# Kernel optimization log

Measured on AMD Instinct MI355X. Metric: run time of the kernel, lower is better.

## Reference

```python
import jax, jax.numpy as jnp
import numpy as np

N_GRAPHS = 128
N_NODES = 512
N = N_GRAPHS * N_NODES      # 65536 total nodes
E = 524288                  # edges (avg degree 8)
F_IN = 4                    # num_features
EMB = 4                     # embedding_dim
HEADS = 4
GDIM = 16                   # GATConv_dim
D = GDIM * HEADS            # 64 = d_model
NHEAD = 2                   # heads // 2
FF = 64                     # ff_hid_dim
OUT = 64                    # output_dim
N_GAT_REST = 3              # gat_layers - 1


def setup_inputs() -> dict:
    key = jax.random.key(0)
    ks = iter(jax.random.split(key, 64))
    def nrm(shape, fan_in):
        return jax.random.normal(next(ks), shape, jnp.float32) / np.float32(np.sqrt(fan_in))
    inp = {}
    inp['x'] = jax.random.normal(next(ks), (N, F_IN), jnp.float32)
    inp['edge_index'] = jax.random.randint(next(ks), (2, E), 0, N, dtype=jnp.int32)
    inp['batch'] = jnp.repeat(jnp.arange(N_GRAPHS, dtype=jnp.int32), N_NODES)
    # feature_fc
    inp['Wf'] = nrm((F_IN, EMB), F_IN); inp['bf'] = jnp.zeros((EMB,), jnp.float32)
    # input GATConv (EMB -> HEADS*GDIM)
    inp['gW0'] = nrm((EMB, HEADS * GDIM), EMB)
    inp['aS0'] = nrm((HEADS, GDIM), GDIM); inp['aD0'] = nrm((HEADS, GDIM), GDIM)
    inp['gb0'] = jnp.zeros((D,), jnp.float32)
    # remaining 3 GATConv layers (D -> HEADS*GDIM), stacked
    inp['gW'] = nrm((N_GAT_REST, D, HEADS * GDIM), D)
    inp['aS'] = nrm((N_GAT_REST, HEADS, GDIM), GDIM); inp['aD'] = nrm((N_GAT_REST, HEADS, GDIM), GDIM)
    inp['gb'] = jnp.zeros((N_GAT_REST, D), jnp.float32)
    # decoder layer: self-attn, cross-attn, layernorms, FFN
    for p in ['sWq','sWk','sWv','sWo','cWq','cWk','cWv','cWo']:
        inp[p] = nrm((D, D), D)
    for p in ['sbq','sbk','sbv','sbo','cbq','cbk','cbv','cbo']:
        inp[p] = jnp.zeros((D,), jnp.float32)
    for g, b in [('ln1g','ln1b'), ('ln2g','ln2b'), ('ln3g','ln3b')]:
        inp[g] = jnp.ones((D,), jnp.float32); inp[b] = jnp.zeros((D,), jnp.float32)
    inp['ffW1'] = nrm((D, FF), D); inp['ffb1'] = jnp.zeros((FF,), jnp.float32)
    inp['ffW2'] = nrm((FF, D), FF); inp['ffb2'] = jnp.zeros((D,), jnp.float32)
    inp['fcW'] = nrm((D, OUT), D); inp['fcb'] = jnp.zeros((OUT,), jnp.float32)
    return inp


def _gat(h_in, src, dst, W, a_s, a_d, b):
    # PyG GATConv, concat=True, negative_slope=0.2, self-loops already in (src,dst)
    h = (h_in @ W).reshape(N, HEADS, GDIM)
    es = jnp.einsum('nho,ho->nh', h, a_s)   # [N,H]
    ed = jnp.einsum('nho,ho->nh', h, a_d)
    e = jax.nn.leaky_relu(es[src] + ed[dst], 0.2)          # [E',H]
    m = jax.ops.segment_max(e, dst, num_segments=N)        # segment softmax over dst
    w = jnp.exp(e - m[dst])
    s = jax.ops.segment_sum(w, dst, num_segments=N)
    alpha = w / (s[dst] + 1e-16)
    out = jax.ops.segment_sum(h[src] * alpha[..., None], dst, num_segments=N)
    return out.reshape(N, D) + b


def _mha(q, kv, Wq, bq, Wk, bk, Wv, bv, Wo, bo):
    B, S, Dm = q.shape
    hd = Dm // NHEAD
    Q = (q @ Wq + bq).reshape(B, S, NHEAD, hd)
    K = (kv @ Wk + bk).reshape(B, S, NHEAD, hd)
    V = (kv @ Wv + bv).reshape(B, S, NHEAD, hd)
    a = jax.nn.softmax(jnp.einsum('bqhd,bkhd->bhqk', Q, K) / jnp.sqrt(jnp.float32(hd)), axis=-1)
    o = jnp.einsum('bhqk,bkhd->bqhd', a, V).reshape(B, S, Dm)
    return o @ Wo + bo


def _ln(x, g, b):
    m = x.mean(-1, keepdims=True)
    v = ((x - m) ** 2).mean(-1, keepdims=True)
    return (x - m) / jnp.sqrt(v + 1e-5) * g + b


def reference(x, edge_index, batch, Wf, bf, gW0, aS0, aD0, gb0, gW, aS, aD, gb,
              sWq, sWk, sWv, sWo, cWq, cWk, cWv, cWo,
              sbq, sbk, sbv, sbo, cbq, cbk, cbv, cbo,
              ln1g, ln1b, ln2g, ln2b, ln3g, ln3b,
              ffW1, ffb1, ffW2, ffb2, fcW, fcb):
    loops = jnp.arange(N, dtype=edge_index.dtype)
    src = jnp.concatenate([edge_index[0], loops])
    dst = jnp.concatenate([edge_index[1], loops])
    h = x @ Wf + bf
    h = jax.nn.leaky_relu(_gat(h, src, dst, gW0, aS0, aD0, gb0), 0.01)
    for i in range(N_GAT_REST):
        h = jax.nn.leaky_relu(_gat(h, src, dst, gW[i], aS[i], aD[i], gb[i]), 0.01)
    t = h.reshape(N_GRAPHS, N_NODES, D)
    # one transformer decoder layer, post-norm, memory = layer input
    mem = t
    t = _ln(t + _mha(t, t, sWq, sbq, sWk, sbk, sWv, sbv, sWo, sbo), ln1g, ln1b)
    t = _ln(t + _mha(t, mem, cWq, cbq, cWk, cbk, cWv, cbv, cWo, cbo), ln2g, ln2b)
    t = _ln(t + (jax.nn.relu(t @ ffW1 + ffb1) @ ffW2 + ffb2), ln3g, ln3b)
    h = t.reshape(N, D)
    pooled = jax.ops.segment_sum(h, batch, num_segments=N_GRAPHS) / jnp.float32(N_NODES)
    return pooled @ fcW + fcb
```

## Files before the change

### kernel.cpp

```cpp
#include <hip/hip_runtime.h>
#include <math.h>

#define NG 128
#define SEQ 512
#define NN 65536
#define EE 524288
#define DM 64

typedef __attribute__((ext_vector_type(8))) short short8;
typedef __attribute__((ext_vector_type(4))) float f32x4;

__device__ __forceinline__ float lrelu(float x, float s){ return x > 0.f ? x : s*x; }

__device__ __forceinline__ unsigned short f2bf(float x){
  union { float f; unsigned u; } v; v.f = x;
  unsigned r = v.u + 0x7FFF + ((v.u>>16)&1);
  return (unsigned short)(r>>16);
}
__device__ __forceinline__ float bf2f(unsigned short x){
  union { unsigned u; float f; } v; v.u = ((unsigned)x)<<16;
  return v.f;
}

__global__ void k_count(const int* __restrict__ dst, int* __restrict__ deg){
  int e = blockIdx.x*256 + threadIdx.x;
  atomicAdd(&deg[dst[e]], 1);
}

__global__ void k_scan1(const int* __restrict__ deg, int* __restrict__ excl, int* __restrict__ bsums){
  __shared__ int sm[256];
  int tid = threadIdx.x;
  int i = blockIdx.x*256 + tid;
  int v = deg[i];
  sm[tid] = v;
  __syncthreads();
  int val = v;
  for (int off=1; off<256; off<<=1){
    int add = (tid>=off)? sm[tid-off] : 0;
    __syncthreads();
    val += add;
    sm[tid] = val;
    __syncthreads();
  }
  excl[i] = val - v;
  if (tid==255) bsums[blockIdx.x] = val;
}

__global__ void k_scan2(int* __restrict__ bsums){
  __shared__ int sm[256];
  int tid=threadIdx.x;
  int v = bsums[tid];
  sm[tid]=v;
  __syncthreads();
  int val=v;
  for (int off=1; off<256; off<<=1){
    int add = (tid>=off)? sm[tid-off]:0;
    __syncthreads();
    val += add;
    sm[tid]=val;
    __syncthreads();
  }
  bsums[tid] = val - v;
}

__global__ void k_scan3(const int* __restrict__ excl, const int* __restrict__ bsums,
                        int* __restrict__ rowp, int* __restrict__ cursor){
  int i = blockIdx.x*256 + threadIdx.x;
  int v = excl[i] + bsums[blockIdx.x];
  rowp[i]=v; cursor[i]=v;
  if (i==0) rowp[NN]=EE;
}

__global__ void k_fill(const int* __restrict__ src, const int* __restrict__ dst,
                       int* __restrict__ cursor, int* __restrict__ col){
  int e = blockIdx.x*256 + threadIdx.x;
  int d = dst[e];
  int p = atomicAdd(&cursor[d], 1);
  col[p] = src[e];
}

__global__ void k_w0(const float* __restrict__ Wf, const float* __restrict__ bf,
                     const float* __restrict__ gW0, float* __restrict__ W0c, float* __restrict__ b0c){
  int j = threadIdx.x;
  float b = 0.f;
  for (int k=0;k<4;k++) b += bf[k]*gW0[k*64+j];
  b0c[j]=b;
  for (int i=0;i<4;i++){
    float s=0.f;
    for(int k=0;k<4;k++) s += Wf[i*4+k]*gW0[k*64+j];
    W0c[i*64+j]=s;
  }
}

template<int DIN, int BIAS>
__global__ void __launch_bounds__(256) k_transform(const float* __restrict__ hin, const float* __restrict__ W,
                            const float* __restrict__ bias,
                            const float* __restrict__ aSp, const float* __restrict__ aDp,
                            unsigned short* __restrict__ hout, float* __restrict__ es, float* __restrict__ ed){
  __shared__ float inL[DIN][68];
  __shared__ float Wl[DIN][64];
  __shared__ float asl[64], adl[64];
  int tid = threadIdx.x;
  int n0 = blockIdx.x*64;
  if (tid < 64){ asl[tid] = aSp[tid]; adl[tid] = aDp[tid]; }
  for (int idx=tid; idx<DIN*16; idx+=256){
    int k = idx>>4, jj = (idx&15)<<2;
    *(float4*)&Wl[k][jj] = *(const float4*)&W[k*64+jj];
  }
  for (int idx=tid; idx<64*(DIN/4); idx+=256){
    int node = idx/(DIN/4), kk = (idx%(DIN/4))*4;
    float4 v = *(const float4*)&hin[(size_t)(n0+node)*DIN + kk];
    inL[kk][node]=v.x; inL[kk+1][node]=v.y; inL[kk+2][node]=v.z; inL[kk+3][node]=v.w;
  }
  __syncthreads();
  int i = tid>>4, j = tid&15;
  float acc[4][4];
  #pragma unroll
  for (int r=0;r<4;r++){
    #pragma unroll
    for (int c=0;c<4;c++) acc[r][c] = 0.f;
  }
  #pragma unroll 4
  for (int k=0;k<DIN;k++){
    float4 av = *(float4*)&inL[k][4*i];
    float4 bv = *(float4*)&Wl[k][4*j];
    float a_[4]={av.x,av.y,av.z,av.w}, b_[4]={bv.x,bv.y,bv.z,bv.w};
    #pragma unroll
    for (int r=0;r<4;r++){
      #pragma unroll
      for (int c=0;c<4;c++) acc[r][c] += a_[r]*b_[c];
    }
  }
  float4 asv = *(float4*)&asl[4*j];
  float4 adv = *(float4*)&adl[4*j];
  float bb[4] = {0.f,0.f,0.f,0.f};
  if (BIAS){
    float4 bv = *(const float4*)&bias[4*j];
    bb[0]=bv.x; bb[1]=bv.y; bb[2]=bv.z; bb[3]=bv.w;
  }
  #pragma unroll
  for (int r=0;r<4;r++){
    float y0=acc[r][0]+bb[0], y1=acc[r][1]+bb[1], y2=acc[r][2]+bb[2], y3=acc[r][3]+bb[3];
    int node = n0 + 4*i + r;
    ushort4 hv;
    hv.x=f2bf(y0); hv.y=f2bf(y1); hv.z=f2bf(y2); hv.w=f2bf(y3);
    *(ushort4*)&hout[(size_t)node*64 + 4*j] = hv;
    float ps = y0*asv.x + y1*asv.y + y2*asv.z + y3*asv.w;
    float pd = y0*adv.x + y1*adv.y + y2*adv.z + y3*adv.w;
    ps += __shfl_xor(ps,1); ps += __shfl_xor(ps,2);
    pd += __shfl_xor(pd,1); pd += __shfl_xor(pd,2);
    if ((j&3)==0){
      es[(size_t)node*4 + (j>>2)] = ps;
      ed[(size_t)node*4 + (j>>2)] = pd;
    }
  }
}

__global__ void __launch_bounds__(256) k_transform_bf(const unsigned short* __restrict__ hin, const float* __restrict__ W,
                            const float* __restrict__ aSp, const float* __restrict__ aDp,
                            unsigned short* __restrict__ hout, float* __restrict__ es, float* __restrict__ ed){
  __shared__ float inL[64][68];
  __shared__ float Wl[64][64];
  __shared__ float asl[64], adl[64];
  int tid = threadIdx.x;
  int n0 = blockIdx.x*64;
  if (tid < 64){ asl[tid] = aSp[tid]; adl[tid] = aDp[tid]; }
  for (int idx=tid; idx<1024; idx+=256){
    int k = idx>>4, jj = (idx&15)<<2;
    *(float4*)&Wl[k][jj] = *(const float4*)&W[k*64+jj];
  }
  for (int idx=tid; idx<1024; idx+=256){
    int node = idx>>4, kk = (idx&15)<<2;
    ushort4 v = *(const ushort4*)&hin[(size_t)(n0+node)*64 + kk];
    inL[kk][node]=bf2f(v.x); inL[kk+1][node]=bf2f(v.y); inL[kk+2][node]=bf2f(v.z); inL[kk+3][node]=bf2f(v.w);
  }
  __syncthreads();
  int i = tid>>4, j = tid&15;
  float acc[4][4];
  #pragma unroll
  for (int r=0;r<4;r++){
    #pragma unroll
    for (int c=0;c<4;c++) acc[r][c] = 0.f;
  }
  #pragma unroll 4
  for (int k=0;k<64;k++){
    float4 av = *(float4*)&inL[k][4*i];
    float4 bv = *(float4*)&Wl[k][4*j];
    float a_[4]={av.x,av.y,av.z,av.w}, b_[4]={bv.x,bv.y,bv.z,bv.w};
    #pragma unroll
    for (int r=0;r<4;r++){
      #pragma unroll
      for (int c=0;c<4;c++) acc[r][c] += a_[r]*b_[c];
    }
  }
  float4 asv = *(float4*)&asl[4*j];
  float4 adv = *(float4*)&adl[4*j];
  #pragma unroll
  for (int r=0;r<4;r++){
    float y0=acc[r][0], y1=acc[r][1], y2=acc[r][2], y3=acc[r][3];
    int node = n0 + 4*i + r;
    ushort4 hv;
    hv.x=f2bf(y0); hv.y=f2bf(y1); hv.z=f2bf(y2); hv.w=f2bf(y3);
    *(ushort4*)&hout[(size_t)node*64 + 4*j] = hv;
    float ps = y0*asv.x + y1*asv.y + y2*asv.z + y3*asv.w;
    float pd = y0*adv.x + y1*adv.y + y2*adv.z + y3*adv.w;
    ps += __shfl_xor(ps,1); ps += __shfl_xor(ps,2);
    pd += __shfl_xor(pd,1); pd += __shfl_xor(pd,2);
    if ((j&3)==0){
      es[(size_t)node*4 + (j>>2)] = ps;
      ed[(size_t)node*4 + (j>>2)] = pd;
    }
  }
}

template<int BF16OUT>
__global__ void __launch_bounds__(256) k_aggregate(const unsigned short* __restrict__ h, const float* __restrict__ es,
                            const float* __restrict__ ed, const int* __restrict__ rowp,
                            const int* __restrict__ col, const float* __restrict__ gb,
                            void* __restrict__ houtv){
  int tid = threadIdx.x;
  int n = blockIdx.x*4 + (tid>>6);
  int l = tid&63;
  int q = l>>4;
  int sl = l&15;
  int head = sl>>2;
  float edn = ed[(size_t)n*4 + head];
  float es_self = es[(size_t)n*4 + head];
  int beg = rowp[n], end = rowp[n+1];
  float m = -1e30f, s = 0.f;
  float a0=0.f, a1=0.f, a2=0.f, a3=0.f;
  for (int i=beg; i<end; i+=8){
    int ei0 = i + q, ei1 = i + 4 + q;
    bool ac0 = ei0 < end, ac1 = ei1 < end;
    int i0 = ac0 ? ei0 : end-1;
    int i1 = ac1 ? ei1 : end-1;
    int s0 = col[i0], s1 = col[i1];
    ushort4 hv0 = *(const ushort4*)&h[(size_t)s0*64 + 4*sl];
    ushort4 hv1 = *(const ushort4*)&h[(size_t)s1*64 + 4*sl];
    float e0 = lrelu(es[(size_t)s0*4+head] + edn, 0.2f);
    float e1 = lrelu(es[(size_t)s1*4+head] + edn, 0.2f);
    if (!ac0) e0 = -1e30f;
    if (!ac1) e1 = -1e30f;
    float mx = fmaxf(e0, e1);
    if (__any(mx > m + 8.f)){
      float nm = fmaxf(m, mx);
      float c = __expf(m - nm);
      s*=c; a0*=c; a1*=c; a2*=c; a3*=c; m = nm;
    }
    float w0 = ac0 ? __expf(e0 - m) : 0.f;
    float w1 = ac1 ? __expf(e1 - m) : 0.f;
    s += w0 + w1;
    a0 += w0*bf2f(hv0.x) + w1*bf2f(hv1.x);
    a1 += w0*bf2f(hv0.y) + w1*bf2f(hv1.y);
    a2 += w0*bf2f(hv0.z) + w1*bf2f(hv1.z);
    a3 += w0*bf2f(hv0.w) + w1*bf2f(hv1.w);
  }
  #pragma unroll
  for (int off=16; off<=32; off<<=1){
    float m2 = __shfl_xor(m, off);
    float s2 = __shfl_xor(s, off);
    float b0 = __shfl_xor(a0, off);
    float b1 = __shfl_xor(a1, off);
    float b2 = __shfl_xor(a2, off);
    float b3 = __shfl_xor(a3, off);
    float nm = fmaxf(m, m2);
    float c1 = __expf(m - nm), c2 = __expf(m2 - nm);
    s  = s*c1  + s2*c2;
    a0 = a0*c1 + b0*c2;
    a1 = a1*c1 + b1*c2;
    a2 = a2*c1 + b2*c2;
    a3 = a3*c1 + b3*c2;
    m = nm;
  }
  {
    float e_self = lrelu(es_self + edn, 0.2f);
    float nm = fmaxf(m, e_self);
    float c = __expf(m - nm), cs = __expf(e_self - nm);
    ushort4 hs = *(const ushort4*)&h[(size_t)n*64 + 4*sl];
    s  = s*c  + cs;
    a0 = a0*c + cs*bf2f(hs.x);
    a1 = a1*c + cs*bf2f(hs.y);
    a2 = a2*c + cs*bf2f(hs.z);
    a3 = a3*c + cs*bf2f(hs.w);
  }
  if (q == 0){
    float inv = 1.f/(s + 1e-16f);
    float4 gv = *(const float4*)&gb[4*sl];
    float o0 = lrelu(a0*inv + gv.x, 0.01f);
    float o1 = lrelu(a1*inv + gv.y, 0.01f);
    float o2 = lrelu(a2*inv + gv.z, 0.01f);
    float o3 = lrelu(a3*inv + gv.w, 0.01f);
    if (BF16OUT){
      ushort4 hv; hv.x=f2bf(o0); hv.y=f2bf(o1); hv.z=f2bf(o2); hv.w=f2bf(o3);
      *(ushort4*)((unsigned short*)houtv + (size_t)n*64 + 4*sl) = hv;
    } else {
      *(float4*)((float*)houtv + (size_t)n*64 + 4*sl) = make_float4(o0,o1,o2,o3);
    }
  }
}

template<int ACT>
__global__ void __launch_bounds__(256) k_linear(const float* __restrict__ in, const float* __restrict__ W,
                         const float* __restrict__ b, float* __restrict__ out){
  __shared__ float inL[64][68];
  __shared__ float Wl[64][64];
  int tid = threadIdx.x;
  int n0 = blockIdx.x*64;
  for (int idx=tid; idx<1024; idx+=256){
    int k = idx>>4, jj = (idx&15)<<2;
    *(float4*)&Wl[k][jj] = *(const float4*)&W[k*64+jj];
  }
  for (int idx=tid; idx<1024; idx+=256){
    int node = idx>>4, kk = (idx&15)<<2;
    float4 v = *(const float4*)&in[(size_t)(n0+node)*64 + kk];
    inL[kk][node]=v.x; inL[kk+1][node]=v.y; inL[kk+2][node]=v.z; inL[kk+3][node]=v.w;
  }
  __syncthreads();
  int i = tid>>4, j = tid&15;
  float acc[4][4];
  #pragma unroll
  for (int r=0;r<4;r++){
    #pragma unroll
    for (int c=0;c<4;c++) acc[r][c] = 0.f;
  }
  #pragma unroll 4
  for (int k=0;k<64;k++){
    float4 av = *(float4*)&inL[k][4*i];
    float4 bv = *(float4*)&Wl[k][4*j];
    float a_[4]={av.x,av.y,av.z,av.w}, b_[4]={bv.x,bv.y,bv.z,bv.w};
    #pragma unroll
    for (int r=0;r<4;r++){
      #pragma unroll
      for (int c=0;c<4;c++) acc[r][c] += a_[r]*b_[c];
    }
  }
  float4 bv = *(const float4*)&b[4*j];
  float bb[4] = {bv.x, bv.y, bv.z, bv.w};
  #pragma unroll
  for (int r=0;r<4;r++){
    float y[4];
    #pragma unroll
    for (int c=0;c<4;c++){
      y[c] = acc[r][c] + bb[c];
      if (ACT==1) y[c] = fmaxf(y[c], 0.f);
    }
    *(float4*)&out[(size_t)(n0+4*i+r)*64 + 4*j] = make_float4(y[0],y[1],y[2],y[3]);
  }
}

__global__ void __launch_bounds__(256) k_qkv3(const float* __restrict__ in0, const float* __restrict__ W0, const float* __restrict__ b0, float* __restrict__ o0,
                      const float* __restrict__ in1, const float* __restrict__ W1, const float* __restrict__ b1, float* __restrict__ o1,
                      const float* __restrict__ in2, const float* __restrict__ W2, const float* __restrict__ b2, float* __restrict__ o2){
  __shared__ float inL[64][68];
  __shared__ float Wl[64][64];
  int tid = threadIdx.x;
  int n0 = blockIdx.x*64;
  int i = tid>>4, j = tid&15;
  const float* ins[3] = {in0, in1, in2};
  const float* Ws[3] = {W0, W1, W2};
  const float* bs[3] = {b0, b1, b2};
  float* os[3] = {o0, o1, o2};
  const float* cur = nullptr;
  for (int w=0; w<3; w++){
    __syncthreads();
    if (ins[w] != cur){
      cur = ins[w];
      for (int idx=tid; idx<1024; idx+=256){
        int node = idx>>4, kk = (idx&15)<<2;
        float4 v = *(const float4*)&cur[(size_t)(n0+node)*64 + kk];
        inL[kk][node]=v.x; inL[kk+1][node]=v.y; inL[kk+2][node]=v.z; inL[kk+3][node]=v.w;
      }
    }
    for (int idx=tid; idx<1024; idx+=256){
      int k = idx>>4, jj = (idx&15)<<2;
      *(float4*)&Wl[k][jj] = *(const float4*)&Ws[w][k*64+jj];
    }
    __syncthreads();
    float acc[4][4];
    #pragma unroll
    for (int r=0;r<4;r++){
      #pragma unroll
      for (int c=0;c<4;c++) acc[r][c] = 0.f;
    }
    #pragma unroll 4
    for (int k=0;k<64;k++){
      float4 av = *(float4*)&inL[k][4*i];
      float4 bv = *(float4*)&Wl[k][4*j];
      float a_[4]={av.x,av.y,av.z,av.w}, b_[4]={bv.x,bv.y,bv.z,bv.w};
      #pragma unroll
      for (int r=0;r<4;r++){
        #pragma unroll
        for (int c=0;c<4;c++) acc[r][c] += a_[r]*b_[c];
      }
    }
    float4 bv = *(const float4*)&bs[w][4*j];
    float bb[4] = {bv.x, bv.y, bv.z, bv.w};
    #pragma unroll
    for (int r=0;r<4;r++){
      *(float4*)&os[w][(size_t)(n0+4*i+r)*64 + 4*j] =
        make_float4(acc[r][0]+bb[0], acc[r][1]+bb[1], acc[r][2]+bb[2], acc[r][3]+bb[3]);
    }
  }
}

__global__ void __launch_bounds__(256) k_linear_resln(const float* __restrict__ in, const float* __restrict__ W,
                               const float* __restrict__ b, const float* __restrict__ res,
                               const float* __restrict__ g, const float* __restrict__ bl,
                               float* __restrict__ out){
  __shared__ float inL[64][68];
  __shared__ float Wl[64][64];
  int tid = threadIdx.x;
  int n0 = blockIdx.x*64;
  for (int idx=tid; idx<1024; idx+=256){
    int k = idx>>4, jj = (idx&15)<<2;
    *(float4*)&Wl[k][jj] = *(const float4*)&W[k*64+jj];
  }
  for (int idx=tid; idx<1024; idx+=256){
    int node = idx>>4, kk = (idx&15)<<2;
    float4 v = *(const float4*)&in[(size_t)(n0+node)*64 + kk];
    inL[kk][node]=v.x; inL[kk+1][node]=v.y; inL[kk+2][node]=v.z; inL[kk+3][node]=v.w;
  }
  __syncthreads();
  int i = tid>>4, j = tid&15;
  float acc[4][4];
  #pragma unroll
  for (int r=0;r<4;r++){
    #pragma unroll
    for (int c=0;c<4;c++) acc[r][c] = 0.f;
  }
  #pragma unroll 4
  for (int k=0;k<64;k++){
    float4 av = *(float4*)&inL[k][4*i];
    float4 bv = *(float4*)&Wl[k][4*j];
    float a_[4]={av.x,av.y,av.z,av.w}, b_[4]={bv.x,bv.y,bv.z,bv.w};
    #pragma unroll
    for (int r=0;r<4;r++){
      #pragma unroll
      for (int c=0;c<4;c++) acc[r][c] += a_[r]*b_[c];
    }
  }
  float4 bv = *(const float4*)&b[4*j];
  float bb[4] = {bv.x, bv.y, bv.z, bv.w};
  float4 gv = *(const float4*)&g[4*j];
  float4 blv = *(const float4*)&bl[4*j];
  float gg[4] = {gv.x, gv.y, gv.z, gv.w};
  float bb2[4] = {blv.x, blv.y, blv.z, blv.w};
  #pragma unroll
  for (int r=0;r<4;r++){
    int node = n0 + 4*i + r;
    float4 rv = *(const float4*)&res[(size_t)node*64 + 4*j];
    float y[4] = {acc[r][0]+bb[0]+rv.x, acc[r][1]+bb[1]+rv.y,
                  acc[r][2]+bb[2]+rv.z, acc[r][3]+bb[3]+rv.w};
    float s = (y[0]+y[1]) + (y[2]+y[3]);
    s += __shfl_xor(s,1); s += __shfl_xor(s,2); s += __shfl_xor(s,4); s += __shfl_xor(s,8);
    float mean = s * (1.f/64.f);
    float d[4] = {y[0]-mean, y[1]-mean, y[2]-mean, y[3]-mean};
    float v = (d[0]*d[0]+d[1]*d[1]) + (d[2]*d[2]+d[3]*d[3]);
    v += __shfl_xor(v,1); v += __shfl_xor(v,2); v += __shfl_xor(v,4); v += __shfl_xor(v,8);
    float inv = rsqrtf(v*(1.f/64.f) + 1e-5f);
    *(float4*)&out[(size_t)node*64 + 4*j] =
      make_float4(d[0]*inv*gg[0]+bb2[0], d[1]*inv*gg[1]+bb2[1],
                  d[2]*inv*gg[2]+bb2[2], d[3]*inv*gg[3]+bb2[3]);
  }
}

__global__ void __launch_bounds__(512, 4) k_attn(const float* __restrict__ Q, const float* __restrict__ K,
                      const float* __restrict__ V, float* __restrict__ Out){
  __shared__ char smem[40960];
  char* Ksm = smem;
  char* Vsm = smem + 16384;
  char* Psm = smem + 32768;

  int bid = blockIdx.x;
  int qh = bid & 1;
  int h  = (bid>>1) & 1;
  int b  = bid>>2;
  int tid = threadIdx.x;
  int wave = tid>>6;
  int l = tid & 63;
  int lq = l & 15;
  int g  = l >> 4;
  const float scale = 0.17677669529663687f;
  const size_t hb = (size_t)b*SEQ*64 + (size_t)h*32;
  const f32x4 zero = {0.f,0.f,0.f,0.f};

  int qbase = qh*256 + wave*32;
  short8 qf[2];
  f32x4 O[2][2];
  float m_[2], l_[2];
  #pragma unroll
  for (int qt=0; qt<2; qt++){
    const float* qp = Q + hb + (size_t)(qbase + qt*16 + lq)*64 + g*8;
    float4 a = *(const float4*)qp;
    float4 c = *(const float4*)(qp+4);
    union { short8 v; unsigned short u[8]; } uu;
    uu.u[0]=f2bf(a.x*scale); uu.u[1]=f2bf(a.y*scale); uu.u[2]=f2bf(a.z*scale); uu.u[3]=f2bf(a.w*scale);
    uu.u[4]=f2bf(c.x*scale); uu.u[5]=f2bf(c.y*scale); uu.u[6]=f2bf(c.z*scale); uu.u[7]=f2bf(c.w*scale);
    qf[qt] = uu.v;
    O[qt][0] = zero; O[qt][1] = zero;
    m_[qt] = -1e30f; l_[qt] = 0.f;
  }

  char* Pw = Psm + wave*1024;

  for (int ph=0; ph<2; ph++){
    __syncthreads();
    #pragma unroll
    for (int it=0; it<4; it++){
      int i = tid + it*512;
      int row = i>>3, j = i&7;
      const float* kp = K + hb + (size_t)(ph*256 + row)*64 + j*4;
      float4 v4 = *(const float4*)kp;
      uint2 w;
      w.x = (unsigned)f2bf(v4.x) | ((unsigned)f2bf(v4.y)<<16);
      w.y = (unsigned)f2bf(v4.z) | ((unsigned)f2bf(v4.w)<<16);
      *(uint2*)(Ksm + row*64 + ((j*8) ^ (((row>>1)&3)<<4))) = w;
    }
    #pragma unroll
    for (int it=0; it<4; it++){
      int i = tid + it*512;
      int key = i>>3, j = i&7;
      const float* vp = V + hb + (size_t)(ph*256 + key)*64 + j*4;
      float4 v4 = *(const float4*)vp;
      float vv[4] = {v4.x, v4.y, v4.z, v4.w};
      #pragma unroll
      for (int c=0;c<4;c++){
        int d = j*4 + c;
        *(unsigned short*)(Vsm + d*512 + ((key*2) ^ ((d&7)<<4))) = f2bf(vv[c]);
      }
    }
    __syncthreads();
    for (int p=0; p<8; p++){
      int r0 = p*32 + lq, r1 = r0 + 16;
      short8 kf0 = *(short8*)(Ksm + r0*64 + ((g*16) ^ (((r0>>1)&3)<<4)));
      short8 kf1 = *(short8*)(Ksm + r1*64 + ((g*16) ^ (((r1>>1)&3)<<4)));
      int d0 = lq, d1 = lq + 16;
      short8 vt0 = *(short8*)(Vsm + d0*512 + ((p*64 + g*16) ^ ((d0&7)<<4)));
      short8 vt1 = *(short8*)(Vsm + d1*512 + ((p*64 + g*16) ^ ((d1&7)<<4)));
      int swzp = ((lq>>1)&3)<<4;
      #pragma unroll
      for (int qt=0; qt<2; qt++){
        f32x4 s0 = __builtin_amdgcn_mfma_f32_16x16x32_bf16(kf0, qf[qt], zero, 0,0,0);
        f32x4 s1 = __builtin_amdgcn_mfma_f32_16x16x32_bf16(kf1, qf[qt], zero, 0,0,0);
        float pmax = fmaxf(fmaxf(fmaxf(s0.x,s0.y),fmaxf(s0.z,s0.w)),
                           fmaxf(fmaxf(s1.x,s1.y),fmaxf(s1.z,s1.w)));
        pmax = fmaxf(pmax, __shfl_xor(pmax, 16));
        pmax = fmaxf(pmax, __shfl_xor(pmax, 32));
        float mn = fmaxf(m_[qt], pmax);
        float corr = __expf(m_[qt] - mn);
        m_[qt] = mn;
        float e0 = __expf(s0.x - mn), e1 = __expf(s0.y - mn);
        float e2 = __expf(s0.z - mn), e3 = __expf(s0.w - mn);
        float e4 = __expf(s1.x - mn), e5 = __expf(s1.y - mn);
        float e6 = __expf(s1.z - mn), e7 = __expf(s1.w - mn);
        l_[qt] = l_[qt]*corr + (((e0+e1)+(e2+e3)) + ((e4+e5)+(e6+e7)));
        O[qt][0] *= corr; O[qt][1] *= corr;
        uint2 w0, w1;
        w0.x = (unsigned)f2bf(e0) | ((unsigned)f2bf(e1)<<16);
        w0.y = (unsigned)f2bf(e2) | ((unsigned)f2bf(e3)<<16);
        w1.x = (unsigned)f2bf(e4) | ((unsigned)f2bf(e5)<<16);
        w1.y = (unsigned)f2bf(e6) | ((unsigned)f2bf(e7)<<16);
        *(uint2*)(Pw + lq*64 + ((g*8) ^ swzp)) = w0;
        *(uint2*)(Pw + lq*64 + ((32 + g*8) ^ swzp)) = w1;
        short8 pb = *(short8*)(Pw + lq*64 + ((g*16) ^ swzp));
        O[qt][0] = __builtin_amdgcn_mfma_f32_16x16x32_bf16(vt0, pb, O[qt][0], 0,0,0);
        O[qt][1] = __builtin_amdgcn_mfma_f32_16x16x32_bf16(vt1, pb, O[qt][1], 0,0,0);
      }
    }
  }
  #pragma unroll
  for (int qt=0; qt<2; qt++){
    float lt = l_[qt];
    lt += __shfl_xor(lt, 16);
    lt += __shfl_xor(lt, 32);
    float inv = 1.f/lt;
    float* op = Out + hb + (size_t)(qbase + qt*16 + lq)*64;
    float4 o0 = make_float4(O[qt][0].x*inv, O[qt][0].y*inv, O[qt][0].z*inv, O[qt][0].w*inv);
    float4 o1 = make_float4(O[qt][1].x*inv, O[qt][1].y*inv, O[qt][1].z*inv, O[qt][1].w*inv);
    *(float4*)(op + g*4) = o0;
    *(float4*)(op + 16 + g*4) = o1;
  }
}

__global__ void __launch_bounds__(256) k_pool_fc(const float* __restrict__ t, const float* __restrict__ fcW,
                          const float* __restrict__ fcb, float* __restrict__ out){
  __shared__ float pl[4][64];
  __shared__ float pf[64];
  int b = blockIdx.x;
  int tid = threadIdx.x;
  int j = tid&63, seg = tid>>6;
  const float* basep = t + (size_t)b*SEQ*64;
  float s = 0.f;
  for (int si=seg*128; si<(seg+1)*128; si++) s += basep[(size_t)si*64 + j];
  pl[seg][j] = s;
  __syncthreads();
  if (tid < 64){
    pf[tid] = (pl[0][tid]+pl[1][tid]+pl[2][tid]+pl[3][tid]) * (1.f/512.f);
  }
  __syncthreads();
  if (tid < 64){
    float o = fcb[tid];
    for (int k=0;k<64;k++) o += pf[k]*fcW[k*64+tid];
    out[(size_t)b*64 + tid] = o;
  }
}

extern "C" void kernel_launch(void* const* d_in, const int* in_sizes, int n_in,
                              void* d_out, int out_size, void* d_ws, size_t ws_size,
                              hipStream_t stream) {
  const float* x    = (const float*)d_in[0];
  const int*   ei   = (const int*)d_in[1];
  const float* Wf   = (const float*)d_in[3];
  const float* bf   = (const float*)d_in[4];
  const float* gW0  = (const float*)d_in[5];
  const float* aS0  = (const float*)d_in[6];
  const float* aD0  = (const float*)d_in[7];
  const float* gb0  = (const float*)d_in[8];
  const float* gW   = (const float*)d_in[9];
  const float* aS   = (const float*)d_in[10];
  const float* aD   = (const float*)d_in[11];
  const float* gb   = (const float*)d_in[12];
  const float* sWq  = (const float*)d_in[13];
  const float* sWk  = (const float*)d_in[14];
  const float* sWv  = (const float*)d_in[15];
  const float* sWo  = (const float*)d_in[16];
  const float* cWq  = (const float*)d_in[17];
  const float* cWk  = (const float*)d_in[18];
  const float* cWv  = (const float*)d_in[19];
  const float* cWo  = (const float*)d_in[20];
  const float* sbq  = (const float*)d_in[21];
  const float* sbk  = (const float*)d_in[22];
  const float* sbv  = (const float*)d_in[23];
  const float* sbo  = (const float*)d_in[24];
  const float* cbq  = (const float*)d_in[25];
  const float* cbk  = (const float*)d_in[26];
  const float* cbv  = (const float*)d_in[27];
  const float* cbo  = (const float*)d_in[28];
  const float* ln1g = (const float*)d_in[29];
  const float* ln1b = (const float*)d_in[30];
  const float* ln2g = (const float*)d_in[31];
  const float* ln2b = (const float*)d_in[32];
  const float* ln3g = (const float*)d_in[33];
  const float* ln3b = (const float*)d_in[34];
  const float* ffW1 = (const float*)d_in[35];
  const float* ffb1 = (const float*)d_in[36];
  const float* ffW2 = (const float*)d_in[37];
  const float* ffb2 = (const float*)d_in[38];
  const float* fcW  = (const float*)d_in[39];
  const float* fcb  = (const float*)d_in[40];

  char* ws = (char*)d_ws;
  size_t off = 0;
  auto alloc = [&](size_t bytes) -> void* {
    void* p = ws + off;
    off += (bytes + 255) & ~(size_t)255;
    return p;
  };
  int* deg    = (int*)alloc(NN*sizeof(int));
  int* excl   = (int*)alloc(NN*sizeof(int));
  int* rowp   = (int*)alloc((NN+1)*sizeof(int));
  int* cursor = (int*)alloc(NN*sizeof(int));
  int* col    = (int*)alloc(EE*sizeof(int));
  int* bsums  = (int*)alloc(256*sizeof(int));
  float* W0c  = (float*)alloc(4*64*sizeof(float));
  float* b0c  = (float*)alloc(64*sizeof(float));
  float* es   = (float*)alloc((size_t)NN*4*sizeof(float));
  float* ed   = (float*)alloc((size_t)NN*4*sizeof(float));
  unsigned short* Hb   = (unsigned short*)alloc((size_t)NN*64*sizeof(unsigned short));
  unsigned short* Hagg = (unsigned short*)alloc((size_t)NN*64*sizeof(unsigned short));
  float* B0   = (float*)alloc((size_t)NN*64*sizeof(float));
  float* B1   = (float*)alloc((size_t)NN*64*sizeof(float));
  float* B2   = (float*)alloc((size_t)NN*64*sizeof(float));
  float* B3   = (float*)alloc((size_t)NN*64*sizeof(float));
  float* B4   = (float*)alloc((size_t)NN*64*sizeof(float));
  float* B5   = (float*)alloc((size_t)NN*64*sizeof(float));

  const int* e_src = ei;
  const int* e_dst = ei + EE;

  hipMemsetAsync(deg, 0, NN*sizeof(int), stream);
  k_count<<<EE/256, 256, 0, stream>>>(e_dst, deg);
  k_scan1<<<NN/256, 256, 0, stream>>>(deg, excl, bsums);
  k_scan2<<<1, 256, 0, stream>>>(bsums);
  k_scan3<<<NN/256, 256, 0, stream>>>(excl, bsums, rowp, cursor);
  k_fill<<<EE/256, 256, 0, stream>>>(e_src, e_dst, cursor, col);

  k_w0<<<1, 64, 0, stream>>>(Wf, bf, gW0, W0c, b0c);

  k_transform<4,1><<<NN/64, 256, 0, stream>>>(x, W0c, b0c, aS0, aD0, Hb, es, ed);
  k_aggregate<1><<<NN/4, 256, 0, stream>>>(Hb, es, ed, rowp, col, gb0, Hagg);
  k_transform_bf<<<NN/64, 256, 0, stream>>>(Hagg, gW+0*4096, aS+0*64, aD+0*64, Hb, es, ed);
  k_aggregate<1><<<NN/4, 256, 0, stream>>>(Hb, es, ed, rowp, col, gb+0*64, Hagg);
  k_transform_bf<<<NN/64, 256, 0, stream>>>(Hagg, gW+1*4096, aS+1*64, aD+1*64, Hb, es, ed);
  k_aggregate<1><<<NN/4, 256, 0, stream>>>(Hb, es, ed, rowp, col, gb+1*64, Hagg);
  k_transform_bf<<<NN/64, 256, 0, stream>>>(Hagg, gW+2*4096, aS+2*64, aD+2*64, Hb, es, ed);
  k_aggregate<0><<<NN/4, 256, 0, stream>>>(Hb, es, ed, rowp, col, gb+2*64, B2);

  k_qkv3<<<NN/64, 256, 0, stream>>>(B2, sWq, sbq, B0, B2, sWk, sbk, B1, B2, sWv, sbv, B3);
  k_attn<<<NG*2*2, 512, 0, stream>>>(B0, B1, B3, B4);
  k_linear_resln<<<NN/64, 256, 0, stream>>>(B4, sWo, sbo, B2, ln1g, ln1b, B5);

  k_qkv3<<<NN/64, 256, 0, stream>>>(B5, cWq, cbq, B0, B2, cWk, cbk, B1, B2, cWv, cbv, B3);
  k_attn<<<NG*2*2, 512, 0, stream>>>(B0, B1, B3, B4);
  k_linear_resln<<<NN/64, 256, 0, stream>>>(B4, cWo, cbo, B5, ln2g, ln2b, B2);

  k_linear<1><<<NN/64, 256, 0, stream>>>(B2, ffW1, ffb1, B0);
  k_linear_resln<<<NN/64, 256, 0, stream>>>(B0, ffW2, ffb2, B2, ln3g, ln3b, B1);

  k_pool_fc<<<NG, 256, 0, stream>>>(B1, fcW, fcb, (float*)d_out);
}
```

Before: 427.1 us.

## Store attention Q/K/V/O in bf16, fuse FFN, restructure GAT edge gather

The QKV projection now writes bf16 outputs with the softmax scale folded into Q. Attention therefore loads bf16 directly, without per-element conversion, and writes bf16 output that the out-projection+LayerNorm kernel reads. The two FFN linears plus the residual LayerNorm are fused into one kernel that keeps the hidden activations in shared memory. The GAT aggregation loop reads 8 consecutive column indices uniformly per iteration, with a separate masked tail, and makes the row bounds wave-uniform. This cuts memory traffic and launches, at the cost of more bf16 rounding on the intermediates.

```diff
diff --git a/kernel.cpp b/kernel.cpp
--- a/kernel.cpp
+++ b/kernel.cpp
@@ -226,19 +226,56 @@
   int head = sl>>2;
   float edn = ed[(size_t)n*4 + head];
   float es_self = es[(size_t)n*4 + head];
-  int beg = rowp[n], end = rowp[n+1];
+  int beg = __builtin_amdgcn_readfirstlane(rowp[n]);
+  int end = __builtin_amdgcn_readfirstlane(rowp[n+1]);
   float m = -1e30f, s = 0.f;
   float a0=0.f, a1=0.f, a2=0.f, a3=0.f;
-  for (int i=beg; i<end; i+=8){
-    int ei0 = i + q, ei1 = i + 4 + q;
-    bool ac0 = ei0 < end, ac1 = ei1 < end;
-    int i0 = ac0 ? ei0 : end-1;
-    int i1 = ac1 ? ei1 : end-1;
-    int s0 = col[i0], s1 = col[i1];
-    ushort4 hv0 = *(const ushort4*)&h[(size_t)s0*64 + 4*sl];
-    ushort4 hv1 = *(const ushort4*)&h[(size_t)s1*64 + 4*sl];
-    float e0 = lrelu(es[(size_t)s0*4+head] + edn, 0.2f);
-    float e1 = lrelu(es[(size_t)s1*4+head] + edn, 0.2f);
+  int i = beg;
+  for (; i+8 <= end; i += 8){
+    int c0=col[i], c1=col[i+1], c2=col[i+2], c3=col[i+3];
+    int c4=col[i+4], c5=col[i+5], c6=col[i+6], c7=col[i+7];
+    int t01 = (q&1)? c1 : c0;
+    int t23 = (q&1)? c3 : c2;
+    int sq0 = (q&2)? t23 : t01;
+    int t45 = (q&1)? c5 : c4;
+    int t67 = (q&1)? c7 : c6;
+    int sq1 = (q&2)? t67 : t45;
+    ushort4 hv0 = *(const ushort4*)&h[(size_t)sq0*64 + 4*sl];
+    ushort4 hv1 = *(const ushort4*)&h[(size_t)sq1*64 + 4*sl];
+    float e0 = lrelu(es[(size_t)sq0*4+head] + edn, 0.2f);
+    float e1 = lrelu(es[(size_t)sq1*4+head] + edn, 0.2f);
+    float mx = fmaxf(e0, e1);
+    if (__any(mx > m + 8.f)){
+      float nm = fmaxf(m, mx);
+      float c = __expf(m - nm);
+      s*=c; a0*=c; a1*=c; a2*=c; a3*=c; m = nm;
+    }
+    float w0 = __expf(e0 - m);
+    float w1 = __expf(e1 - m);
+    s += w0 + w1;
+    a0 += w0*bf2f(hv0.x) + w1*bf2f(hv1.x);
+    a1 += w0*bf2f(hv0.y) + w1*bf2f(hv1.y);
+    a2 += w0*bf2f(hv0.z) + w1*bf2f(hv1.z);
+    a3 += w0*bf2f(hv0.w) + w1*bf2f(hv1.w);
+  }
+  if (i < end){
+    int last = end-1;
+    int i1=(i+1<last)?i+1:last, i2=(i+2<last)?i+2:last, i3=(i+3<last)?i+3:last;
+    int i4=(i+4<last)?i+4:last, i5=(i+5<last)?i+5:last, i6=(i+6<last)?i+6:last;
+    int c0=col[i], c1=col[i1], c2=col[i2], c3=col[i3];
+    int c4=col[i4], c5=col[i5], c6=col[i6], c7=col[last];
+    int t01 = (q&1)? c1 : c0;
+    int t23 = (q&1)? c3 : c2;
+    int sq0 = (q&2)? t23 : t01;
+    int t45 = (q&1)? c5 : c4;
+    int t67 = (q&1)? c7 : c6;
+    int sq1 = (q&2)? t67 : t45;
+    bool ac0 = (i + q) < end;
+    bool ac1 = (i + 4 + q) < end;
+    ushort4 hv0 = *(const ushort4*)&h[(size_t)sq0*64 + 4*sl];
+    ushort4 hv1 = *(const ushort4*)&h[(size_t)sq1*64 + 4*sl];
+    float e0 = lrelu(es[(size_t)sq0*4+head] + edn, 0.2f);
+    float e1 = lrelu(es[(size_t)sq1*4+head] + edn, 0.2f);
     if (!ac0) e0 = -1e30f;
     if (!ac1) e1 = -1e30f;
     float mx = fmaxf(e0, e1);
@@ -299,58 +336,10 @@
   }
 }
 
-template<int ACT>
-__global__ void __launch_bounds__(256) k_linear(const float* __restrict__ in, const float* __restrict__ W,
-                         const float* __restrict__ b, float* __restrict__ out){
-  __shared__ float inL[64][68];
-  __shared__ float Wl[64][64];
-  int tid = threadIdx.x;
-  int n0 = blockIdx.x*64;
-  for (int idx=tid; idx<1024; idx+=256){
-    int k = idx>>4, jj = (idx&15)<<2;
-    *(float4*)&Wl[k][jj] = *(const float4*)&W[k*64+jj];
-  }
-  for (int idx=tid; idx<1024; idx+=256){
-    int node = idx>>4, kk = (idx&15)<<2;
-    float4 v = *(const float4*)&in[(size_t)(n0+node)*64 + kk];
-    inL[kk][node]=v.x; inL[kk+1][node]=v.y; inL[kk+2][node]=v.z; inL[kk+3][node]=v.w;
-  }
-  __syncthreads();
-  int i = tid>>4, j = tid&15;
-  float acc[4][4];
-  #pragma unroll
-  for (int r=0;r<4;r++){
-    #pragma unroll
-    for (int c=0;c<4;c++) acc[r][c] = 0.f;
-  }
-  #pragma unroll 4
-  for (int k=0;k<64;k++){
-    float4 av = *(float4*)&inL[k][4*i];
-    float4 bv = *(float4*)&Wl[k][4*j];
-    float a_[4]={av.x,av.y,av.z,av.w}, b_[4]={bv.x,bv.y,bv.z,bv.w};
-    #pragma unroll
-    for (int r=0;r<4;r++){
-      #pragma unroll
-      for (int c=0;c<4;c++) acc[r][c] += a_[r]*b_[c];
-    }
-  }
-  float4 bv = *(const float4*)&b[4*j];
-  float bb[4] = {bv.x, bv.y, bv.z, bv.w};
-  #pragma unroll
-  for (int r=0;r<4;r++){
-    float y[4];
-    #pragma unroll
-    for (int c=0;c<4;c++){
-      y[c] = acc[r][c] + bb[c];
-      if (ACT==1) y[c] = fmaxf(y[c], 0.f);
-    }
-    *(float4*)&out[(size_t)(n0+4*i+r)*64 + 4*j] = make_float4(y[0],y[1],y[2],y[3]);
-  }
-}
-
-__global__ void __launch_bounds__(256) k_qkv3(const float* __restrict__ in0, const float* __restrict__ W0, const float* __restrict__ b0, float* __restrict__ o0,
-                      const float* __restrict__ in1, const float* __restrict__ W1, const float* __restrict__ b1, float* __restrict__ o1,
-                      const float* __restrict__ in2, const float* __restrict__ W2, const float* __restrict__ b2, float* __restrict__ o2){
+__global__ void __launch_bounds__(256) k_qkv3(const float* __restrict__ in0, const float* __restrict__ W0, const float* __restrict__ b0, unsigned short* __restrict__ o0,
+                      const float* __restrict__ in1, const float* __restrict__ W1, const float* __restrict__ b1, unsigned short* __restrict__ o1,
+                      const float* __restrict__ in2, const float* __restrict__ W2, const float* __restrict__ b2, unsigned short* __restrict__ o2,
+                      float scl0){
   __shared__ float inL[64][68];
   __shared__ float Wl[64][64];
   int tid = threadIdx.x;
@@ -359,7 +348,7 @@
   const float* ins[3] = {in0, in1, in2};
   const float* Ws[3] = {W0, W1, W2};
   const float* bs[3] = {b0, b1, b2};
-  float* os[3] = {o0, o1, o2};
+  unsigned short* os[3] = {o0, o1, o2};
   const float* cur = nullptr;
   for (int w=0; w<3; w++){
     __syncthreads();
@@ -395,15 +384,20 @@
     }
     float4 bv = *(const float4*)&bs[w][4*j];
     float bb[4] = {bv.x, bv.y, bv.z, bv.w};
+    float sc = (w==0) ? scl0 : 1.f;
     #pragma unroll
     for (int r=0;r<4;r++){
-      *(float4*)&os[w][(size_t)(n0+4*i+r)*64 + 4*j] =
-        make_float4(acc[r][0]+bb[0], acc[r][1]+bb[1], acc[r][2]+bb[2], acc[r][3]+bb[3]);
-    }
-  }
-}
-
-__global__ void __launch_bounds__(256) k_linear_resln(const float* __restrict__ in, const float* __restrict__ W,
+      ushort4 hv;
+      hv.x = f2bf((acc[r][0]+bb[0])*sc);
+      hv.y = f2bf((acc[r][1]+bb[1])*sc);
+      hv.z = f2bf((acc[r][2]+bb[2])*sc);
+      hv.w = f2bf((acc[r][3]+bb[3])*sc);
+      *(ushort4*)&os[w][(size_t)(n0+4*i+r)*64 + 4*j] = hv;
+    }
+  }
+}
+
+__global__ void __launch_bounds__(256) k_resln_bf(const unsigned short* __restrict__ in, const float* __restrict__ W,
                                const float* __restrict__ b, const float* __restrict__ res,
                                const float* __restrict__ g, const float* __restrict__ bl,
                                float* __restrict__ out){
@@ -417,8 +411,8 @@
   }
   for (int idx=tid; idx<1024; idx+=256){
     int node = idx>>4, kk = (idx&15)<<2;
-    float4 v = *(const float4*)&in[(size_t)(n0+node)*64 + kk];
-    inL[kk][node]=v.x; inL[kk+1][node]=v.y; inL[kk+2][node]=v.z; inL[kk+3][node]=v.w;
+    ushort4 v = *(const ushort4*)&in[(size_t)(n0+node)*64 + kk];
+    inL[kk][node]=bf2f(v.x); inL[kk+1][node]=bf2f(v.y); inL[kk+2][node]=bf2f(v.z); inL[kk+3][node]=bf2f(v.w);
   }
   __syncthreads();
   int i = tid>>4, j = tid&15;
@@ -464,8 +458,102 @@
   }
 }
 
-__global__ void __launch_bounds__(512, 4) k_attn(const float* __restrict__ Q, const float* __restrict__ K,
-                      const float* __restrict__ V, float* __restrict__ Out){
+__global__ void __launch_bounds__(256) k_ffn(const float* __restrict__ in,
+                     const float* __restrict__ W1p, const float* __restrict__ b1p,
+                     const float* __restrict__ W2p, const float* __restrict__ b2p,
+                     const float* __restrict__ g, const float* __restrict__ bl,
+                     float* __restrict__ out){
+  __shared__ float inL[64][68];
+  __shared__ float Wl[64][64];
+  __shared__ float ffL[64][68];
+  int tid = threadIdx.x;
+  int n0 = blockIdx.x*64;
+  for (int idx=tid; idx<1024; idx+=256){
+    int k = idx>>4, jj = (idx&15)<<2;
+    *(float4*)&Wl[k][jj] = *(const float4*)&W1p[k*64+jj];
+  }
+  for (int idx=tid; idx<1024; idx+=256){
+    int node = idx>>4, kk = (idx&15)<<2;
+    float4 v = *(const float4*)&in[(size_t)(n0+node)*64 + kk];
+    inL[kk][node]=v.x; inL[kk+1][node]=v.y; inL[kk+2][node]=v.z; inL[kk+3][node]=v.w;
+  }
+  __syncthreads();
+  int i = tid>>4, j = tid&15;
+  float acc[4][4];
+  #pragma unroll
+  for (int r=0;r<4;r++){
+    #pragma unroll
+    for (int c=0;c<4;c++) acc[r][c] = 0.f;
+  }
+  #pragma unroll 4
+  for (int k=0;k<64;k++){
+    float4 av = *(float4*)&inL[k][4*i];
+    float4 bv = *(float4*)&Wl[k][4*j];
+    float a_[4]={av.x,av.y,av.z,av.w}, b_[4]={bv.x,bv.y,bv.z,bv.w};
+    #pragma unroll
+    for (int r=0;r<4;r++){
+      #pragma unroll
+      for (int c=0;c<4;c++) acc[r][c] += a_[r]*b_[c];
+    }
+  }
+  float4 b1v = *(const float4*)&b1p[4*j];
+  float bb1[4] = {b1v.x, b1v.y, b1v.z, b1v.w};
+  #pragma unroll
+  for (int r=0;r<4;r++){
+    #pragma unroll
+    for (int c=0;c<4;c++){
+      ffL[4*j+c][4*i+r] = fmaxf(acc[r][c] + bb1[c], 0.f);
+    }
+  }
+  __syncthreads();
+  for (int idx=tid; idx<1024; idx+=256){
+    int k = idx>>4, jj = (idx&15)<<2;
+    *(float4*)&Wl[k][jj] = *(const float4*)&W2p[k*64+jj];
+  }
+  __syncthreads();
+  #pragma unroll
+  for (int r=0;r<4;r++){
+    #pragma unroll
+    for (int c=0;c<4;c++) acc[r][c] = 0.f;
+  }
+  #pragma unroll 4
+  for (int k=0;k<64;k++){
+    float4 av = *(float4*)&ffL[k][4*i];
+    float4 bv = *(float4*)&Wl[k][4*j];
+    float a_[4]={av.x,av.y,av.z,av.w}, b_[4]={bv.x,bv.y,bv.z,bv.w};
+    #pragma unroll
+    for (int r=0;r<4;r++){
+      #pragma unroll
+      for (int c=0;c<4;c++) acc[r][c] += a_[r]*b_[c];
+    }
+  }
+  float4 b2v = *(const float4*)&b2p[4*j];
+  float bb2v[4] = {b2v.x, b2v.y, b2v.z, b2v.w};
+  float4 gv = *(const float4*)&g[4*j];
+  float4 blv = *(const float4*)&bl[4*j];
+  float gg[4] = {gv.x, gv.y, gv.z, gv.w};
+  float bbl[4] = {blv.x, blv.y, blv.z, blv.w};
+  #pragma unroll
+  for (int r=0;r<4;r++){
+    int node = n0 + 4*i + r;
+    float y[4];
+    #pragma unroll
+    for (int c=0;c<4;c++) y[c] = acc[r][c] + bb2v[c] + inL[4*j+c][4*i+r];
+    float s = (y[0]+y[1]) + (y[2]+y[3]);
+    s += __shfl_xor(s,1); s += __shfl_xor(s,2); s += __shfl_xor(s,4); s += __shfl_xor(s,8);
+    float mean = s * (1.f/64.f);
+    float d[4] = {y[0]-mean, y[1]-mean, y[2]-mean, y[3]-mean};
+    float v = (d[0]*d[0]+d[1]*d[1]) + (d[2]*d[2]+d[3]*d[3]);
+    v += __shfl_xor(v,1); v += __shfl_xor(v,2); v += __shfl_xor(v,4); v += __shfl_xor(v,8);
+    float inv = rsqrtf(v*(1.f/64.f) + 1e-5f);
+    *(float4*)&out[(size_t)node*64 + 4*j] =
+      make_float4(d[0]*inv*gg[0]+bbl[0], d[1]*inv*gg[1]+bbl[1],
+                  d[2]*inv*gg[2]+bbl[2], d[3]*inv*gg[3]+bbl[3]);
+  }
+}
+
+__global__ void __launch_bounds__(512, 4) k_attn(const unsigned short* __restrict__ Q, const unsigned short* __restrict__ K,
+                      const unsigned short* __restrict__ V, unsigned short* __restrict__ Out){
   __shared__ char smem[40960];
   char* Ksm = smem;
   char* Vsm = smem + 16384;
@@ -480,7 +568,6 @@
   int l = tid & 63;
   int lq = l & 15;
   int g  = l >> 4;
-  const float scale = 0.17677669529663687f;
   const size_t hb = (size_t)b*SEQ*64 + (size_t)h*32;
   const f32x4 zero = {0.f,0.f,0.f,0.f};
 
@@ -490,13 +577,7 @@
   float m_[2], l_[2];
   #pragma unroll
   for (int qt=0; qt<2; qt++){
-    const float* qp = Q + hb + (size_t)(qbase + qt*16 + lq)*64 + g*8;
-    float4 a = *(const float4*)qp;
-    float4 c = *(const float4*)(qp+4);
-    union { short8 v; unsigned short u[8]; } uu;
-    uu.u[0]=f2bf(a.x*scale); uu.u[1]=f2bf(a.y*scale); uu.u[2]=f2bf(a.z*scale); uu.u[3]=f2bf(a.w*scale);
-    uu.u[4]=f2bf(c.x*scale); uu.u[5]=f2bf(c.y*scale); uu.u[6]=f2bf(c.z*scale); uu.u[7]=f2bf(c.w*scale);
-    qf[qt] = uu.v;
+    qf[qt] = *(const short8*)(Q + hb + (size_t)(qbase + qt*16 + lq)*64 + g*8);
     O[qt][0] = zero; O[qt][1] = zero;
     m_[qt] = -1e30f; l_[qt] = 0.f;
   }
@@ -506,27 +587,22 @@
   for (int ph=0; ph<2; ph++){
     __syncthreads();
     #pragma unroll
-    for (int it=0; it<4; it++){
+    for (int it=0; it<2; it++){
       int i = tid + it*512;
-      int row = i>>3, j = i&7;
-      const float* kp = K + hb + (size_t)(ph*256 + row)*64 + j*4;
-      float4 v4 = *(const float4*)kp;
-      uint2 w;
-      w.x = (unsigned)f2bf(v4.x) | ((unsigned)f2bf(v4.y)<<16);
-      w.y = (unsigned)f2bf(v4.z) | ((unsigned)f2bf(v4.w)<<16);
-      *(uint2*)(Ksm + row*64 + ((j*8) ^ (((row>>1)&3)<<4))) = w;
-    }
-    #pragma unroll
-    for (int it=0; it<4; it++){
+      int row = i>>2, j = i&3;
+      uint4 v = *(const uint4*)(K + hb + (size_t)(ph*256 + row)*64 + j*8);
+      *(uint4*)(Ksm + row*64 + ((j*16) ^ (((row>>1)&3)<<4))) = v;
+    }
+    #pragma unroll
+    for (int it=0; it<2; it++){
       int i = tid + it*512;
-      int key = i>>3, j = i&7;
-      const float* vp = V + hb + (size_t)(ph*256 + key)*64 + j*4;
-      float4 v4 = *(const float4*)vp;
-      float vv[4] = {v4.x, v4.y, v4.z, v4.w};
-      #pragma unroll
-      for (int c=0;c<4;c++){
-        int d = j*4 + c;
-        *(unsigned short*)(Vsm + d*512 + ((key*2) ^ ((d&7)<<4))) = f2bf(vv[c]);
+      int key = i>>2, j = i&3;
+      uint4 vv = *(const uint4*)(V + hb + (size_t)(ph*256 + key)*64 + j*8);
+      const unsigned short* vs = (const unsigned short*)&vv;
+      #pragma unroll
+      for (int c=0;c<8;c++){
+        int d = j*8 + c;
+        *(unsigned short*)(Vsm + d*512 + ((key*2) ^ ((d&7)<<4))) = vs[c];
       }
     }
     __syncthreads();
@@ -574,11 +650,12 @@
     lt += __shfl_xor(lt, 16);
     lt += __shfl_xor(lt, 32);
     float inv = 1.f/lt;
-    float* op = Out + hb + (size_t)(qbase + qt*16 + lq)*64;
-    float4 o0 = make_float4(O[qt][0].x*inv, O[qt][0].y*inv, O[qt][0].z*inv, O[qt][0].w*inv);
-    float4 o1 = make_float4(O[qt][1].x*inv, O[qt][1].y*inv, O[qt][1].z*inv, O[qt][1].w*inv);
-    *(float4*)(op + g*4) = o0;
-    *(float4*)(op + 16 + g*4) = o1;
+    unsigned short* op = Out + hb + (size_t)(qbase + qt*16 + lq)*64;
+    ushort4 o0, o1;
+    o0.x=f2bf(O[qt][0].x*inv); o0.y=f2bf(O[qt][0].y*inv); o0.z=f2bf(O[qt][0].z*inv); o0.w=f2bf(O[qt][0].w*inv);
+    o1.x=f2bf(O[qt][1].x*inv); o1.y=f2bf(O[qt][1].y*inv); o1.z=f2bf(O[qt][1].z*inv); o1.w=f2bf(O[qt][1].w*inv);
+    *(ushort4*)(op + g*4) = o0;
+    *(ushort4*)(op + 16 + g*4) = o1;
   }
 }
 
@@ -668,15 +745,18 @@
   float* ed   = (float*)alloc((size_t)NN*4*sizeof(float));
   unsigned short* Hb   = (unsigned short*)alloc((size_t)NN*64*sizeof(unsigned short));
   unsigned short* Hagg = (unsigned short*)alloc((size_t)NN*64*sizeof(unsigned short));
-  float* B0   = (float*)alloc((size_t)NN*64*sizeof(float));
+  unsigned short* Qb = (unsigned short*)alloc((size_t)NN*64*sizeof(unsigned short));
+  unsigned short* Kb = (unsigned short*)alloc((size_t)NN*64*sizeof(unsigned short));
+  unsigned short* Vb = (unsigned short*)alloc((size_t)NN*64*sizeof(unsigned short));
+  unsigned short* Ob = (unsigned short*)alloc((size_t)NN*64*sizeof(unsigned short));
   float* B1   = (float*)alloc((size_t)NN*64*sizeof(float));
   float* B2   = (float*)alloc((size_t)NN*64*sizeof(float));
-  float* B3   = (float*)alloc((size_t)NN*64*sizeof(float));
-  float* B4   = (float*)alloc((size_t)NN*64*sizeof(float));
   float* B5   = (float*)alloc((size_t)NN*64*sizeof(float));
 
   const int* e_src = ei;
   const int* e_dst = ei + EE;
+
+  const float scale = 0.17677669529663687f;
 
   hipMemsetAsync(deg, 0, NN*sizeof(int), stream);
   k_count<<<EE/256, 256, 0, stream>>>(e_dst, deg);
@@ -696,16 +776,15 @@
   k_transform_bf<<<NN/64, 256, 0, stream>>>(Hagg, gW+2*4096, aS+2*64, aD+2*64, Hb, es, ed);
   k_aggregate<0><<<NN/4, 256, 0, stream>>>(Hb, es, ed, rowp, col, gb+2*64, B2);
 
-  k_qkv3<<<NN/64, 256, 0, stream>>>(B2, sWq, sbq, B0, B2, sWk, sbk, B1, B2, sWv, sbv, B3);
-  k_attn<<<NG*2*2, 512, 0, stream>>>(B0, B1, B3, B4);
-  k_linear_resln<<<NN/64, 256, 0, stream>>>(B4, sWo, sbo, B2, ln1g, ln1b, B5);
-
-  k_qkv3<<<NN/64, 256, 0, stream>>>(B5, cWq, cbq, B0, B2, cWk, cbk, B1, B2, cWv, cbv, B3);
-  k_attn<<<NG*2*2, 512, 0, stream>>>(B0, B1, B3, B4);
-  k_linear_resln<<<NN/64, 256, 0, stream>>>(B4, cWo, cbo, B5, ln2g, ln2b, B2);
-
-  k_linear<1><<<NN/64, 256, 0, stream>>>(B2, ffW1, ffb1, B0);
-  k_linear_resln<<<NN/64, 256, 0, stream>>>(B0, ffW2, ffb2, B2, ln3g, ln3b, B1);
+  k_qkv3<<<NN/64, 256, 0, stream>>>(B2, sWq, sbq, Qb, B2, sWk, sbk, Kb, B2, sWv, sbv, Vb, scale);
+  k_attn<<<NG*2*2, 512, 0, stream>>>(Qb, Kb, Vb, Ob);
+  k_resln_bf<<<NN/64, 256, 0, stream>>>(Ob, sWo, sbo, B2, ln1g, ln1b, B5);
+
+  k_qkv3<<<NN/64, 256, 0, stream>>>(B5, cWq, cbq, Qb, B2, cWk, cbk, Kb, B2, cWv, cbv, Vb, scale);
+  k_attn<<<NG*2*2, 512, 0, stream>>>(Qb, Kb, Vb, Ob);
+  k_resln_bf<<<NN/64, 256, 0, stream>>>(Ob, cWo, cbo, B5, ln2g, ln2b, B2);
+
+  k_ffn<<<NN/64, 256, 0, stream>>>(B2, ffW1, ffb1, ffW2, ffb2, ln3g, ln3b, B1);
 
   k_pool_fc<<<NG, 256, 0, stream>>>(B1, fcW, fcb, (float*)d_out);
 }
```

Result: faster. 409.4 us (-4.2%).
